# Performance work log

Hardware: AMD Instinct MI355X
Metric: run time of the kernel (lower is better)

Reference implementation:

```python
import jax, jax.numpy as jnp
import numpy as np

N_NODES = 40000
N_EDGES = 640000
D_IN = 128
D_HID = 128
D_OUT = 128
N_GRAPHS = 128


def setup_inputs() -> dict:
    key = jax.random.key(0)
    ks = jax.random.split(key, 12)
    x = jax.random.normal(ks[0], (N_NODES, D_IN), dtype=jnp.float32)
    edge_index = jax.random.randint(ks[1], (2, N_EDGES), 0, N_NODES, dtype=jnp.int64)
    batch = jnp.sort(jax.random.randint(ks[2], (N_NODES,), 0, N_GRAPHS, dtype=jnp.int64))
    def lin(k, fan_in, shape):
        s = 1.0 / np.sqrt(fan_in)
        return jax.random.uniform(k, shape, dtype=jnp.float32, minval=-s, maxval=s)
    return {
        "x": x, "edge_index": edge_index, "batch": batch,
        "W_rel0": lin(ks[3], D_IN, (D_IN, D_HID)), "b_rel0": lin(ks[4], D_IN, (D_HID,)), "W_root0": lin(ks[5], D_IN, (D_IN, D_HID)),
        "W_rel1": lin(ks[6], D_HID, (D_HID, D_HID)), "b_rel1": lin(ks[7], D_HID, (D_HID,)), "W_root1": lin(ks[8], D_HID, (D_HID, D_HID)),
        "W_rel2": lin(ks[9], D_HID, (D_HID, D_OUT)), "b_rel2": lin(ks[10], D_HID, (D_OUT,)), "W_root2": lin(ks[11], D_HID, (D_HID, D_OUT)),
    }


def graph_conv(x, src, dst, W_rel, b_rel, W_root):
    # PyG GraphConv: out_i = Lin_rel(sum_{j in N(i)} x_j) + Lin_root(x_i)
    agg = jax.ops.segment_sum(x[src], dst, num_segments=N_NODES)  # [N, F]
    return agg @ W_rel + b_rel + x @ W_root


def reference(x, edge_index, batch,
              W_rel0, b_rel0, W_root0,
              W_rel1, b_rel1, W_root1,
              W_rel2, b_rel2, W_root2):
    src, dst = edge_index[0], edge_index[1]
    h = graph_conv(x, src, dst, W_rel0, b_rel0, W_root0)
    h = jax.nn.relu(h)  # dropout is identity in eval mode
    h = graph_conv(h, src, dst, W_rel1, b_rel1, W_root1)
    h = jax.nn.relu(h)
    h = graph_conv(h, src, dst, W_rel2, b_rel2, W_root2)
    # global_max_pool over per-node graph ids -> [n_graphs, D_OUT]
    return jax.ops.segment_max(h, batch, num_segments=N_GRAPHS)
```

## Files before the change

kernel.cpp:

```cpp
#include <hip/hip_runtime.h>
#include <hip/hip_bf16.h>
#include <math.h>

#define N_NODES 40000
#define N_EDGES 640000
#define D 128
#define N_GRAPHS 128
#define SCAN_NBLK ((N_NODES + 255) / 256)
#define LDS_STRIDE 68

typedef __attribute__((ext_vector_type(8))) short bf16x8;
typedef __attribute__((ext_vector_type(4))) float f32x4;
typedef __attribute__((ext_vector_type(4))) unsigned int u32x4;
typedef unsigned int __attribute__((address_space(3))) lds_u32;
typedef unsigned int __attribute__((address_space(1))) glb_u32;

static __device__ __forceinline__ unsigned short f2b(float f) {
    unsigned int u = __float_as_uint(f);
    unsigned int r = (u + 0x7fffu + ((u >> 16) & 1u)) >> 16;
    return (unsigned short)r;
}
static __device__ __forceinline__ float blo(unsigned int u) {
    return __uint_as_float(u << 16);
}
static __device__ __forceinline__ float bhi(unsigned int u) {
    return __uint_as_float(u & 0xffff0000u);
}
static __device__ __forceinline__ unsigned int fkey(float x) {
    unsigned int b = __float_as_uint(x);
    return (b & 0x80000000u) ? ~b : (b | 0x80000000u);
}

__global__ void __launch_bounds__(256) k_init(
    int* __restrict__ counts,
    unsigned short* __restrict__ xb, unsigned short* __restrict__ hA,
    unsigned short* __restrict__ hB, unsigned int* __restrict__ outk) {
    int n = blockIdx.x * 256 + threadIdx.x;
    if (n < N_GRAPHS * D) outk[n] = 0x007FFFFFu;
    if (n < N_NODES) counts[n] = 0;
    if (blockIdx.x == SCAN_NBLK) {
        int t = threadIdx.x;
        if (t < 48) {
            int row = t >> 4, c = t & 15;
            unsigned short* p = (row == 0) ? xb : (row == 1) ? hA : hB;
            u32x4 z = {0u, 0u, 0u, 0u};
            ((u32x4*)(p + (size_t)N_NODES * D))[c] = z;
        }
    }
}

__global__ void __launch_bounds__(256) k_pack1(
    const int* __restrict__ ei, int* __restrict__ counts,
    const float* __restrict__ x, unsigned int* __restrict__ xb,
    const float* __restrict__ Wr0, const float* __restrict__ Wt0,
    const float* __restrict__ Wr1, const float* __restrict__ Wt1,
    const float* __restrict__ Wr2, const float* __restrict__ Wt2,
    unsigned short* __restrict__ WT) {
    int b = blockIdx.x;
    int t = threadIdx.x;
    if (b < 2500) {
        int e = b * 256 + t;
        atomicAdd(&counts[ei[N_EDGES + e]], 1);
    } else if (b < 5000) {
        int i = (b - 2500) * 256 + t;
        const f32x4* xv = (const f32x4*)x;
        f32x4 v0 = xv[i * 2], v1 = xv[i * 2 + 1];
        u32x4 o;
        o.x = ((unsigned int)f2b(v0.y) << 16) | f2b(v0.x);
        o.y = ((unsigned int)f2b(v0.w) << 16) | f2b(v0.z);
        o.z = ((unsigned int)f2b(v1.y) << 16) | f2b(v1.x);
        o.w = ((unsigned int)f2b(v1.w) << 16) | f2b(v1.z);
        ((u32x4*)xb)[i] = o;
    } else {
        int bw = b - 5000;
        int l = bw >> 7, c = bw & 127, k = t;
        const float* Wrel = (l == 0) ? Wr0 : (l == 1) ? Wr1 : Wr2;
        const float* Wroot = (l == 0) ? Wt0 : (l == 1) ? Wt1 : Wt2;
        float v = (k < D) ? Wrel[k * D + c] : Wroot[(k - D) * D + c];
        WT[(size_t)l * 128 * 256 + c * 256 + k] = f2b(v);
    }
}

__global__ void __launch_bounds__(256) k_scan1(const int* __restrict__ counts,
                                               int* __restrict__ local_pre,
                                               int* __restrict__ blocksums) {
    int t = threadIdx.x;
    int i = blockIdx.x * 256 + t;
    int lane = t & 63, wave = t >> 6;
    int v = (i < N_NODES) ? ((counts[i] + 15) & ~15) : 0;
    int incl = v;
#pragma unroll
    for (int off = 1; off < 64; off <<= 1) {
        int u = __shfl_up(incl, off);
        if (lane >= off) incl += u;
    }
    __shared__ int ws[4];
    if (lane == 63) ws[wave] = incl;
    __syncthreads();
    int base = 0;
    for (int w = 0; w < 4; ++w) {
        int s = ws[w];
        if (w < wave) base += s;
    }
    if (i < N_NODES) local_pre[i] = base + incl - v;
    if (t == 255) blocksums[blockIdx.x] = base + incl;
}

__global__ void __launch_bounds__(256) k_scan3(const int* __restrict__ local_pre,
                                               const int* __restrict__ blocksums,
                                               const int* __restrict__ counts,
                                               int* __restrict__ rp_pad,
                                               int* __restrict__ cursor,
                                               int* __restrict__ src_pad) {
    int t = threadIdx.x;
    int lane = t & 63, wave = t >> 6;
    int bid = blockIdx.x;
    int v = (t < bid) ? blocksums[t] : 0;
#pragma unroll
    for (int off = 32; off >= 1; off >>= 1) v += __shfl_xor(v, off);
    __shared__ int ws[4];
    if (lane == 0) ws[wave] = v;
    __syncthreads();
    int base = ws[0] + ws[1] + ws[2] + ws[3];

    int i = bid * 256 + t;
    if (i < N_NODES) {
        int rp = base + local_pre[i];
        rp_pad[i] = rp;
        cursor[i] = rp;
        int c = counts[i];
        int pc = (c + 15) & ~15;
        for (int j = rp + c; j < rp + pc; ++j) src_pad[j] = N_NODES;
        if (i == N_NODES - 1) rp_pad[N_NODES] = rp + pc;
    }
}

__global__ void k_scatter(const int* __restrict__ ei, int* __restrict__ cursor,
                          int* __restrict__ src_pad) {
    int e = blockIdx.x * blockDim.x + threadIdx.x;
    if (e < N_EDGES) {
        int d = ei[N_EDGES + e];
        int pos = atomicAdd(&cursor[d], 1);
        src_pad[pos] = ei[e];
    }
}

__global__ void __launch_bounds__(256) k_layer(
    const unsigned short* __restrict__ in,
    const int* __restrict__ rp_pad,
    const int* __restrict__ src_pad,
    const unsigned short* __restrict__ WT,
    const float* __restrict__ bias,
    unsigned short* __restrict__ out,
    const int* __restrict__ batch,
    unsigned int* __restrict__ outk) {
    __shared__ __align__(1024) char stage[4][2][4096];
    __shared__ __align__(16) unsigned int aggLDS[16 * LDS_STRIDE];

    int tid = threadIdx.x;
    int w = tid >> 6;
    int lane = tid & 63;
    int nodebase = blockIdx.x * 16;

    const int* rp = rp_pad + nodebase + w * 4;
    int r0 = rp[0], r1 = rp[1], r2 = rp[2], r3 = rp[3], r4 = rp[4];

    int hh = lane >> 4;
    int cc = lane & 15;
    const char* inb = (const char*)in;
    unsigned gofs = 16u * (unsigned)cc;

#define STAGE4(BI, I0, I1, I2, I3) do {                                        \
        __builtin_amdgcn_global_load_lds(                                      \
            (const glb_u32*)(inb + (((size_t)(unsigned)(I0)) << 8) + gofs),    \
            (lds_u32*)&stage[w][BI][0], 16, 0, 0);                             \
        __builtin_amdgcn_global_load_lds(                                      \
            (const glb_u32*)(inb + (((size_t)(unsigned)(I1)) << 8) + gofs),    \
            (lds_u32*)&stage[w][BI][1024], 16, 0, 0);                          \
        __builtin_amdgcn_global_load_lds(                                      \
            (const glb_u32*)(inb + (((size_t)(unsigned)(I2)) << 8) + gofs),    \
            (lds_u32*)&stage[w][BI][2048], 16, 0, 0);                          \
        __builtin_amdgcn_global_load_lds(                                      \
            (const glb_u32*)(inb + (((size_t)(unsigned)(I3)) << 8) + gofs),    \
            (lds_u32*)&stage[w][BI][3072], 16, 0, 0);                          \
    } while (0)

#define ACC8(v) do { \
        a0 += blo((v).x); a1 += bhi((v).x); \
        a2 += blo((v).y); a3 += bhi((v).y); \
        a4 += blo((v).z); a5 += bhi((v).z); \
        a6 += blo((v).w); a7 += bhi((v).w); } while (0)

    int i0 = 0, i1 = 0, i2 = 0, i3 = 0;
    int pos = r0;
    int buf_i = 0, buf_c = 0;
    if (pos < r4) {
        i0 = src_pad[pos + hh];       i1 = src_pad[pos + 4 + hh];
        i2 = src_pad[pos + 8 + hh];   i3 = src_pad[pos + 12 + hh];
        STAGE4(0, i0, i1, i2, i3);
        buf_i = 1;
        pos += 16;
        if (pos < r4) {
            i0 = src_pad[pos + hh];       i1 = src_pad[pos + 4 + hh];
            i2 = src_pad[pos + 8 + hh];   i3 = src_pad[pos + 12 + hh];
        }
    }

#pragma unroll
    for (int n = 0; n < 4; ++n) {
        int ps = (n == 0) ? r0 : (n == 1) ? r1 : (n == 2) ? r2 : r3;
        int pe = (n == 0) ? r1 : (n == 1) ? r2 : (n == 2) ? r3 : r4;
        float a0 = 0.f, a1 = 0.f, a2 = 0.f, a3 = 0.f;
        float a4 = 0.f, a5 = 0.f, a6 = 0.f, a7 = 0.f;
        for (int p = ps; p < pe; p += 16) {
            asm volatile("s_waitcnt vmcnt(0)" ::: "memory");
            if (pos < r4) {
                STAGE4(buf_i, i0, i1, i2, i3);
                buf_i ^= 1;
                pos += 16;
                if (pos < r4) {
                    i0 = src_pad[pos + hh];       i1 = src_pad[pos + 4 + hh];
                    i2 = src_pad[pos + 8 + hh];   i3 = src_pad[pos + 12 + hh];
                }
            }
            const u32x4* sb = (const u32x4*)&stage[w][buf_c][0];
            u32x4 v0 = sb[0 * 64 + lane];
            u32x4 v1 = sb[1 * 64 + lane];
            u32x4 v2 = sb[2 * 64 + lane];
            u32x4 v3 = sb[3 * 64 + lane];
            ACC8(v0); ACC8(v1); ACC8(v2); ACC8(v3);
            buf_c ^= 1;
        }
#define RED(a) do { a += __shfl_xor(a, 16); a += __shfl_xor(a, 32); } while (0)
        RED(a0); RED(a1); RED(a2); RED(a3);
        RED(a4); RED(a5); RED(a6); RED(a7);
#undef RED
        if (lane < 16) {
            u32x4 o;
            o.x = ((unsigned int)f2b(a1) << 16) | f2b(a0);
            o.y = ((unsigned int)f2b(a3) << 16) | f2b(a2);
            o.z = ((unsigned int)f2b(a5) << 16) | f2b(a4);
            o.w = ((unsigned int)f2b(a7) << 16) | f2b(a6);
            *(u32x4*)&aggLDS[(w * 4 + n) * LDS_STRIDE + 4 * cc] = o;
        }
    }
#undef STAGE4
#undef ACC8
    __syncthreads();

    int row = cc, quad = hh;
    int colbase = w * 32;

    f32x4 gacc0 = {0.f, 0.f, 0.f, 0.f};
    f32x4 gacc1 = {0.f, 0.f, 0.f, 0.f};

    const unsigned int* Al = &aggLDS[row * LDS_STRIDE];
    const short* Xp = (const short*)(in + (nodebase + row) * D);
    const short* W0 = (const short*)(WT + (colbase + row) * 256);
    const short* W1 = (const short*)(WT + (colbase + 16 + row) * 256);

#pragma unroll
    for (int t = 0; t < 4; ++t) {
        bf16x8 af = *(const bf16x8*)(Al + t * 16 + quad * 4);
        int k0 = t * 32 + quad * 8;
        bf16x8 b0 = *(const bf16x8*)(W0 + k0);
        bf16x8 b1 = *(const bf16x8*)(W1 + k0);
        gacc0 = __builtin_amdgcn_mfma_f32_16x16x32_bf16(af, b0, gacc0, 0, 0, 0);
        gacc1 = __builtin_amdgcn_mfma_f32_16x16x32_bf16(af, b1, gacc1, 0, 0, 0);
    }
#pragma unroll
    for (int t = 0; t < 4; ++t) {
        int k0 = t * 32 + quad * 8;
        bf16x8 xf = *(const bf16x8*)(Xp + k0);
        bf16x8 b0 = *(const bf16x8*)(W0 + 128 + k0);
        bf16x8 b1 = *(const bf16x8*)(W1 + 128 + k0);
        gacc0 = __builtin_amdgcn_mfma_f32_16x16x32_bf16(xf, b0, gacc0, 0, 0, 0);
        gacc1 = __builtin_amdgcn_mfma_f32_16x16x32_bf16(xf, b1, gacc1, 0, 0, 0);
    }

    int c0 = colbase + row, c1 = c0 + 16;
    float bia0 = bias[c0], bia1 = bias[c1];
    float v0[4], v1[4];
#pragma unroll
    for (int r = 0; r < 4; ++r) { v0[r] = gacc0[r] + bia0; v1[r] = gacc1[r] + bia1; }

    if (outk == nullptr) {
#pragma unroll
        for (int r = 0; r < 4; ++r) {
            int n2 = nodebase + quad * 4 + r;
            out[n2 * D + c0] = f2b(fmaxf(v0[r], 0.f));
            out[n2 * D + c1] = f2b(fmaxf(v1[r], 0.f));
        }
    } else {
        int g0 = batch[nodebase];
        int g15 = batch[nodebase + 15];
        if (g0 == g15) {
            float m0 = fmaxf(fmaxf(v0[0], v0[1]), fmaxf(v0[2], v0[3]));
            float m1 = fmaxf(fmaxf(v1[0], v1[1]), fmaxf(v1[2], v1[3]));
            m0 = fmaxf(m0, __shfl_xor(m0, 16)); m0 = fmaxf(m0, __shfl_xor(m0, 32));
            m1 = fmaxf(m1, __shfl_xor(m1, 16)); m1 = fmaxf(m1, __shfl_xor(m1, 32));
            if (quad == 0) {
                atomicMax(&outk[g0 * D + c0], fkey(m0));
                atomicMax(&outk[g0 * D + c1], fkey(m1));
            }
        } else {
#pragma unroll
            for (int r = 0; r < 4; ++r) {
                int gg = batch[nodebase + quad * 4 + r];
                atomicMax(&outk[gg * D + c0], fkey(v0[r]));
                atomicMax(&outk[gg * D + c1], fkey(v1[r]));
            }
        }
    }
}

__global__ void k_unmap(unsigned int* __restrict__ outk) {
    int i = blockIdx.x * 256 + threadIdx.x;
    unsigned int k = outk[i];
    unsigned int b = (k & 0x80000000u) ? (k ^ 0x80000000u) : ~k;
    ((float*)outk)[i] = __uint_as_float(b);
}

extern "C" void kernel_launch(void* const* d_in, const int* in_sizes, int n_in,
                              void* d_out, int out_size, void* d_ws, size_t ws_size,
                              hipStream_t stream) {
    const float* x = (const float*)d_in[0];
    const int* ei = (const int*)d_in[1];
    const int* batch = (const int*)d_in[2];
    const float* Wrel[3]  = {(const float*)d_in[3], (const float*)d_in[6], (const float*)d_in[9]};
    const float* brel[3]  = {(const float*)d_in[4], (const float*)d_in[7], (const float*)d_in[10]};
    const float* Wroot[3] = {(const float*)d_in[5], (const float*)d_in[8], (const float*)d_in[11]};
    unsigned int* outk = (unsigned int*)d_out;

    char* ws = (char*)d_ws;
    size_t off = 0;
    auto alloc = [&](size_t bytes) -> void* {
        void* p = ws + off;
        off = (off + bytes + 255) & ~(size_t)255;
        return p;
    };
    unsigned short* xb  = (unsigned short*)alloc((size_t)(N_NODES + 1) * D * 2);
    unsigned short* hA  = (unsigned short*)alloc((size_t)(N_NODES + 1) * D * 2);
    unsigned short* hB  = (unsigned short*)alloc((size_t)(N_NODES + 1) * D * 2);
    unsigned short* WT  = (unsigned short*)alloc((size_t)3 * 128 * 256 * 2);
    int* rp_pad     = (int*)alloc((size_t)(N_NODES + 1) * 4);
    int* counts     = (int*)alloc((size_t)N_NODES * 4);
    int* cursor     = (int*)alloc((size_t)N_NODES * 4);
    int* src_pad    = (int*)alloc((size_t)(N_EDGES + 16 * N_NODES) * 4);
    int* local_pre  = (int*)alloc((size_t)N_NODES * 4);
    int* blocksums  = (int*)alloc((size_t)SCAN_NBLK * 4);

    k_init<<<SCAN_NBLK + 1, 256, 0, stream>>>(counts, xb, hA, hB, outk);
    k_pack1<<<5384, 256, 0, stream>>>(ei, counts, x, (unsigned int*)xb,
                                      Wrel[0], Wroot[0], Wrel[1], Wroot[1],
                                      Wrel[2], Wroot[2], WT);
    k_scan1<<<SCAN_NBLK, 256, 0, stream>>>(counts, local_pre, blocksums);
    k_scan3<<<SCAN_NBLK, 256, 0, stream>>>(local_pre, blocksums, counts,
                                           rp_pad, cursor, src_pad);
    k_scatter<<<(N_EDGES + 255) / 256, 256, 0, stream>>>(ei, cursor, src_pad);

    k_layer<<<N_NODES / 16, 256, 0, stream>>>(xb, rp_pad, src_pad, WT,
                                              brel[0], hA, batch, nullptr);
    k_layer<<<N_NODES / 16, 256, 0, stream>>>(hA, rp_pad, src_pad, WT + 128 * 256,
                                              brel[1], hB, batch, nullptr);
    k_layer<<<N_NODES / 16, 256, 0, stream>>>(hB, rp_pad, src_pad, WT + 2 * 128 * 256,
                                              brel[2], hB, batch, outk);

    k_unmap<<<N_GRAPHS * D / 256, 256, 0, stream>>>(outk);
}
```

Before: 283.9 us.

## Gather neighbor features in fp8 to halve aggregation traffic

Each layer now also writes an fp8 (e4m3) copy of its activations, and the neighbor gather-sum reads 128-byte fp8 rows instead of 256-byte bf16 rows. The root term and the GEMM still use bf16. The aim is to halve the bytes moved by the irregular gather, which dominates each layer. The cost is much lower precision in the aggregated sums, which may exceed the accuracy tolerance, plus an extra fp8 write pass, LDS staging and two block syncs in the epilogue.

```diff
diff --git a/kernel.cpp b/kernel.cpp
--- a/kernel.cpp
+++ b/kernel.cpp
@@ -11,7 +11,9 @@
 
 typedef __attribute__((ext_vector_type(8))) short bf16x8;
 typedef __attribute__((ext_vector_type(4))) float f32x4;
+typedef __attribute__((ext_vector_type(2))) float f32x2;
 typedef __attribute__((ext_vector_type(4))) unsigned int u32x4;
+typedef __attribute__((ext_vector_type(2))) unsigned int u32x2;
 typedef unsigned int __attribute__((address_space(3))) lds_u32;
 typedef unsigned int __attribute__((address_space(1))) glb_u32;
 
@@ -20,30 +22,33 @@
     unsigned int r = (u + 0x7fffu + ((u >> 16) & 1u)) >> 16;
     return (unsigned short)r;
 }
-static __device__ __forceinline__ float blo(unsigned int u) {
-    return __uint_as_float(u << 16);
-}
-static __device__ __forceinline__ float bhi(unsigned int u) {
-    return __uint_as_float(u & 0xffff0000u);
-}
 static __device__ __forceinline__ unsigned int fkey(float x) {
     unsigned int b = __float_as_uint(x);
     return (b & 0x80000000u) ? ~b : (b | 0x80000000u);
 }
+static __device__ __forceinline__ unsigned int f2p8(float f) {
+    return __builtin_amdgcn_cvt_pk_fp8_f32(f, 0.f, 0, false) & 0xffu;
+}
 
 __global__ void __launch_bounds__(256) k_init(
     int* __restrict__ counts,
     unsigned short* __restrict__ xb, unsigned short* __restrict__ hA,
-    unsigned short* __restrict__ hB, unsigned int* __restrict__ outk) {
+    unsigned short* __restrict__ hB,
+    unsigned char* __restrict__ x8, unsigned char* __restrict__ h8A,
+    unsigned char* __restrict__ h8B, unsigned int* __restrict__ outk) {
     int n = blockIdx.x * 256 + threadIdx.x;
     if (n < N_GRAPHS * D) outk[n] = 0x007FFFFFu;
     if (n < N_NODES) counts[n] = 0;
     if (blockIdx.x == SCAN_NBLK) {
         int t = threadIdx.x;
+        u32x4 z = {0u, 0u, 0u, 0u};
         if (t < 48) {
             int row = t >> 4, c = t & 15;
             unsigned short* p = (row == 0) ? xb : (row == 1) ? hA : hB;
-            u32x4 z = {0u, 0u, 0u, 0u};
+            ((u32x4*)(p + (size_t)N_NODES * D))[c] = z;
+        } else if (t < 72) {
+            int row = (t - 48) >> 3, c = (t - 48) & 7;
+            unsigned char* p = (row == 0) ? x8 : (row == 1) ? h8A : h8B;
             ((u32x4*)(p + (size_t)N_NODES * D))[c] = z;
         }
     }
@@ -52,6 +57,7 @@
 __global__ void __launch_bounds__(256) k_pack1(
     const int* __restrict__ ei, int* __restrict__ counts,
     const float* __restrict__ x, unsigned int* __restrict__ xb,
+    unsigned char* __restrict__ x8,
     const float* __restrict__ Wr0, const float* __restrict__ Wt0,
     const float* __restrict__ Wr1, const float* __restrict__ Wt1,
     const float* __restrict__ Wr2, const float* __restrict__ Wt2,
@@ -71,6 +77,12 @@
         o.z = ((unsigned int)f2b(v1.y) << 16) | f2b(v1.x);
         o.w = ((unsigned int)f2b(v1.w) << 16) | f2b(v1.z);
         ((u32x4*)xb)[i] = o;
+        unsigned p0 = __builtin_amdgcn_cvt_pk_fp8_f32(v0.x, v0.y, 0, false);
+        p0 = __builtin_amdgcn_cvt_pk_fp8_f32(v0.z, v0.w, p0, true);
+        unsigned p1 = __builtin_amdgcn_cvt_pk_fp8_f32(v1.x, v1.y, 0, false);
+        p1 = __builtin_amdgcn_cvt_pk_fp8_f32(v1.z, v1.w, p1, true);
+        u32x2 o8; o8.x = p0; o8.y = p1;
+        ((u32x2*)x8)[i] = o8;
     } else {
         int bw = b - 5000;
         int l = bw >> 7, c = bw & 127, k = t;
@@ -147,14 +159,16 @@
 
 __global__ void __launch_bounds__(256) k_layer(
     const unsigned short* __restrict__ in,
+    const unsigned char* __restrict__ in8,
     const int* __restrict__ rp_pad,
     const int* __restrict__ src_pad,
     const unsigned short* __restrict__ WT,
     const float* __restrict__ bias,
     unsigned short* __restrict__ out,
+    unsigned char* __restrict__ out8,
     const int* __restrict__ batch,
     unsigned int* __restrict__ outk) {
-    __shared__ __align__(1024) char stage[4][2][4096];
+    __shared__ __align__(1024) char stage[4][2][2048];
     __shared__ __align__(16) unsigned int aggLDS[16 * LDS_STRIDE];
 
     int tid = threadIdx.x;
@@ -167,42 +181,31 @@
 
     int hh = lane >> 4;
     int cc = lane & 15;
-    const char* inb = (const char*)in;
-    unsigned gofs = 16u * (unsigned)cc;
-
-#define STAGE4(BI, I0, I1, I2, I3) do {                                        \
+    int j8 = lane >> 3;
+    const char* in8b = (const char*)in8;
+    unsigned gofs8 = 16u * (unsigned)(lane & 7);
+
+#define STAGE2(BI, IA, IB) do {                                                \
         __builtin_amdgcn_global_load_lds(                                      \
-            (const glb_u32*)(inb + (((size_t)(unsigned)(I0)) << 8) + gofs),    \
+            (const glb_u32*)(in8b + (((size_t)(unsigned)(IA)) << 7) + gofs8),  \
             (lds_u32*)&stage[w][BI][0], 16, 0, 0);                             \
         __builtin_amdgcn_global_load_lds(                                      \
-            (const glb_u32*)(inb + (((size_t)(unsigned)(I1)) << 8) + gofs),    \
+            (const glb_u32*)(in8b + (((size_t)(unsigned)(IB)) << 7) + gofs8),  \
             (lds_u32*)&stage[w][BI][1024], 16, 0, 0);                          \
-        __builtin_amdgcn_global_load_lds(                                      \
-            (const glb_u32*)(inb + (((size_t)(unsigned)(I2)) << 8) + gofs),    \
-            (lds_u32*)&stage[w][BI][2048], 16, 0, 0);                          \
-        __builtin_amdgcn_global_load_lds(                                      \
-            (const glb_u32*)(inb + (((size_t)(unsigned)(I3)) << 8) + gofs),    \
-            (lds_u32*)&stage[w][BI][3072], 16, 0, 0);                          \
     } while (0)
 
-#define ACC8(v) do { \
-        a0 += blo((v).x); a1 += bhi((v).x); \
-        a2 += blo((v).y); a3 += bhi((v).y); \
-        a4 += blo((v).z); a5 += bhi((v).z); \
-        a6 += blo((v).w); a7 += bhi((v).w); } while (0)
-
-    int i0 = 0, i1 = 0, i2 = 0, i3 = 0;
+    int ia = 0, ib = 0;
     int pos = r0;
     int buf_i = 0, buf_c = 0;
     if (pos < r4) {
-        i0 = src_pad[pos + hh];       i1 = src_pad[pos + 4 + hh];
-        i2 = src_pad[pos + 8 + hh];   i3 = src_pad[pos + 12 + hh];
-        STAGE4(0, i0, i1, i2, i3);
+        ia = src_pad[pos + j8];
+        ib = src_pad[pos + 8 + j8];
+        STAGE2(0, ia, ib);
         buf_i = 1;
         pos += 16;
         if (pos < r4) {
-            i0 = src_pad[pos + hh];       i1 = src_pad[pos + 4 + hh];
-            i2 = src_pad[pos + 8 + hh];   i3 = src_pad[pos + 12 + hh];
+            ia = src_pad[pos + j8];
+            ib = src_pad[pos + 8 + j8];
         }
     }
 
@@ -215,20 +218,25 @@
         for (int p = ps; p < pe; p += 16) {
             asm volatile("s_waitcnt vmcnt(0)" ::: "memory");
             if (pos < r4) {
-                STAGE4(buf_i, i0, i1, i2, i3);
+                STAGE2(buf_i, ia, ib);
                 buf_i ^= 1;
                 pos += 16;
                 if (pos < r4) {
-                    i0 = src_pad[pos + hh];       i1 = src_pad[pos + 4 + hh];
-                    i2 = src_pad[pos + 8 + hh];   i3 = src_pad[pos + 12 + hh];
+                    ia = src_pad[pos + j8];
+                    ib = src_pad[pos + 8 + j8];
                 }
             }
-            const u32x4* sb = (const u32x4*)&stage[w][buf_c][0];
-            u32x4 v0 = sb[0 * 64 + lane];
-            u32x4 v1 = sb[1 * 64 + lane];
-            u32x4 v2 = sb[2 * 64 + lane];
-            u32x4 v3 = sb[3 * 64 + lane];
-            ACC8(v0); ACC8(v1); ACC8(v2); ACC8(v3);
+            const char* sb = &stage[w][buf_c][0];
+#pragma unroll
+            for (int pp = 0; pp < 4; ++pp) {
+                u32x2 dv = *(const u32x2*)(sb + 512 * pp + 128 * hh + 8 * cc);
+                f32x2 l0 = __builtin_amdgcn_cvt_pk_f32_fp8(dv.x, false);
+                f32x2 h0 = __builtin_amdgcn_cvt_pk_f32_fp8(dv.x, true);
+                f32x2 l1 = __builtin_amdgcn_cvt_pk_f32_fp8(dv.y, false);
+                f32x2 h1 = __builtin_amdgcn_cvt_pk_f32_fp8(dv.y, true);
+                a0 += l0.x; a1 += l0.y; a2 += h0.x; a3 += h0.y;
+                a4 += l1.x; a5 += l1.y; a6 += h1.x; a7 += h1.y;
+            }
             buf_c ^= 1;
         }
 #define RED(a) do { a += __shfl_xor(a, 16); a += __shfl_xor(a, 32); } while (0)
@@ -244,8 +252,7 @@
             *(u32x4*)&aggLDS[(w * 4 + n) * LDS_STRIDE + 4 * cc] = o;
         }
     }
-#undef STAGE4
-#undef ACC8
+#undef STAGE2
     __syncthreads();
 
     int row = cc, quad = hh;
@@ -288,8 +295,24 @@
 #pragma unroll
         for (int r = 0; r < 4; ++r) {
             int n2 = nodebase + quad * 4 + r;
-            out[n2 * D + c0] = f2b(fmaxf(v0[r], 0.f));
-            out[n2 * D + c1] = f2b(fmaxf(v1[r], 0.f));
+            float r0v = fmaxf(v0[r], 0.f), r1v = fmaxf(v1[r], 0.f);
+            out[n2 * D + c0] = f2b(r0v);
+            out[n2 * D + c1] = f2b(r1v);
+            v0[r] = r0v; v1[r] = r1v;
+        }
+        __syncthreads();
+        unsigned char* agg8 = (unsigned char*)aggLDS;
+#pragma unroll
+        for (int r = 0; r < 4; ++r) {
+            int n2l = quad * 4 + r;
+            agg8[n2l * 128 + c0] = (unsigned char)f2p8(v0[r]);
+            agg8[n2l * 128 + c1] = (unsigned char)f2p8(v1[r]);
+        }
+        __syncthreads();
+        if (tid < 128) {
+            int nl = tid >> 3, co = (tid & 7) * 16;
+            *(u32x4*)(out8 + (size_t)(nodebase + nl) * D + co) =
+                *(const u32x4*)(agg8 + nl * 128 + co);
         }
     } else {
         int g0 = batch[nodebase];
@@ -342,6 +365,9 @@
     unsigned short* xb  = (unsigned short*)alloc((size_t)(N_NODES + 1) * D * 2);
     unsigned short* hA  = (unsigned short*)alloc((size_t)(N_NODES + 1) * D * 2);
     unsigned short* hB  = (unsigned short*)alloc((size_t)(N_NODES + 1) * D * 2);
+    unsigned char* x8   = (unsigned char*)alloc((size_t)(N_NODES + 1) * D);
+    unsigned char* h8A  = (unsigned char*)alloc((size_t)(N_NODES + 1) * D);
+    unsigned char* h8B  = (unsigned char*)alloc((size_t)(N_NODES + 1) * D);
     unsigned short* WT  = (unsigned short*)alloc((size_t)3 * 128 * 256 * 2);
     int* rp_pad     = (int*)alloc((size_t)(N_NODES + 1) * 4);
     int* counts     = (int*)alloc((size_t)N_NODES * 4);
@@ -350,8 +376,8 @@
     int* local_pre  = (int*)alloc((size_t)N_NODES * 4);
     int* blocksums  = (int*)alloc((size_t)SCAN_NBLK * 4);
 
-    k_init<<<SCAN_NBLK + 1, 256, 0, stream>>>(counts, xb, hA, hB, outk);
-    k_pack1<<<5384, 256, 0, stream>>>(ei, counts, x, (unsigned int*)xb,
+    k_init<<<SCAN_NBLK + 1, 256, 0, stream>>>(counts, xb, hA, hB, x8, h8A, h8B, outk);
+    k_pack1<<<5384, 256, 0, stream>>>(ei, counts, x, (unsigned int*)xb, x8,
                                       Wrel[0], Wroot[0], Wrel[1], Wroot[1],
                                       Wrel[2], Wroot[2], WT);
     k_scan1<<<SCAN_NBLK, 256, 0, stream>>>(counts, local_pre, blocksums);
@@ -359,12 +385,12 @@
                                            rp_pad, cursor, src_pad);
     k_scatter<<<(N_EDGES + 255) / 256, 256, 0, stream>>>(ei, cursor, src_pad);
 
-    k_layer<<<N_NODES / 16, 256, 0, stream>>>(xb, rp_pad, src_pad, WT,
-                                              brel[0], hA, batch, nullptr);
-    k_layer<<<N_NODES / 16, 256, 0, stream>>>(hA, rp_pad, src_pad, WT + 128 * 256,
-                                              brel[1], hB, batch, nullptr);
-    k_layer<<<N_NODES / 16, 256, 0, stream>>>(hB, rp_pad, src_pad, WT + 2 * 128 * 256,
-                                              brel[2], hB, batch, outk);
+    k_layer<<<N_NODES / 16, 256, 0, stream>>>(xb, x8, rp_pad, src_pad, WT,
+                                              brel[0], hA, h8A, batch, nullptr);
+    k_layer<<<N_NODES / 16, 256, 0, stream>>>(hA, h8A, rp_pad, src_pad, WT + 128 * 256,
+                                              brel[1], hB, h8B, batch, nullptr);
+    k_layer<<<N_NODES / 16, 256, 0, stream>>>(hB, h8B, rp_pad, src_pad, WT + 2 * 128 * 256,
+                                              brel[2], hB, h8B, batch, outk);
 
     k_unmap<<<N_GRAPHS * D / 256, 256, 0, stream>>>(outk);
 }
```

After: 266.1 us, median of 2. 6.3% less time.
